# Optimization experiments

Hardware: AMD Instinct MI355X
Metric: run time of the kernel (lower is better)

## Reference

```python
import jax, jax.numpy as jnp
import numpy as np

INPUT_SIZE = 1024
HIDDEN = 4096
NUM_BLOCKS = 8
BLOCK = HIDDEN // NUM_BLOCKS  # 512
T, B = 64, 256


def setup_inputs() -> dict:
    key = jax.random.key(0)
    ks = jax.random.split(key, 5)
    stdv = 1.0 / np.sqrt(HIDDEN)
    x = jax.random.normal(ks[0], (T, B, INPUT_SIZE), dtype=jnp.float32)
    h_0 = jnp.zeros((B, HIDDEN), dtype=jnp.float32)
    # nn.Linear(input_size, 3*hidden): weight (3H, in), bias (3H)
    W_i_w = jax.random.uniform(ks[1], (3 * HIDDEN, INPUT_SIZE), minval=-stdv, maxval=stdv, dtype=jnp.float32)
    W_i_b = jax.random.uniform(ks[2], (3 * HIDDEN,), minval=-stdv, maxval=stdv, dtype=jnp.float32)
    # per-block nn.Linear(block, 3*block, bias=False): weight (3s, s), stacked (nb, 3s, s)
    W_h = jax.random.uniform(ks[3], (NUM_BLOCKS, 3 * BLOCK, BLOCK), minval=-stdv, maxval=stdv, dtype=jnp.float32)
    b_h = jax.random.uniform(ks[4], (3 * HIDDEN,), minval=-stdv, maxval=stdv, dtype=jnp.float32)
    return {"x": x, "h_0": h_0, "W_i_w": W_i_w, "W_i_b": W_i_b, "W_h": W_h, "b_h": b_h}


def reference(x, h_0, W_i_w, W_i_b, W_h, b_h):
    Tt, Bb, _ = x.shape
    H = b_h.shape[0] // 3
    nb = W_h.shape[0]
    s = H // nb
    # precompute input gates for all timesteps: (T, B, 3H)
    x_gates = jnp.einsum('tbi,gi->tbg', x, W_i_w) + W_i_b

    def step(h, xg):
        # block-diagonal recurrent transform; layout per block is [r_b, z_b, n_b] (3s),
        # concatenated over blocks -> (B, 3H) interleaved, matching torch cat order
        hb = h.reshape(Bb, nb, s)
        h_gates = jnp.einsum('bns,ngs->bng', hb, W_h).reshape(Bb, 3 * H) + b_h
        gates = xg + h_gates
        # torch chunk(3, dim=1) slices by H (mixes gate types across blocks -- faithful)
        r_t = jax.nn.sigmoid(gates[:, :H])
        z_t = jax.nn.sigmoid(gates[:, H:2 * H])
        h_n_gate = h_gates[:, 2 * H:]
        x_n_gate = xg[:, 2 * H:]
        n_t = jnp.tanh(x_n_gate + r_t * h_n_gate)
        h_new = (1.0 - z_t) * n_t + z_t * h
        return h_new, h_new

    h_T, output = jax.lax.scan(step, h_0, x_gates)
    return output, h_T
```

## Files before the change

### kernel.cpp

```cpp
#include <hip/hip_runtime.h>

#define T_STEPS 64
#define BATCH   256
#define IN_SZ   1024
#define HID     4096
#define BLK     512
#define GATES   12288
#define GROW    1536

#define BM 128
#define BN 128
#define BK 64

using bf16x8  = __attribute__((ext_vector_type(8))) __bf16;
using floatx4 = __attribute__((ext_vector_type(4))) float;
typedef const __attribute__((address_space(1))) unsigned int* gas_u32;
typedef __attribute__((address_space(3))) unsigned int* las_u32;

__device__ __forceinline__ unsigned short f2bf(float f) {
    union { float f; unsigned int u; } v; v.f = f;
    unsigned int u = v.u;
    unsigned int r = (u + 0x7fffu + ((u >> 16) & 1u)) >> 16;
    return (unsigned short)r;
}

__global__ __launch_bounds__(256) void cast_f32_bf16(
    const float* __restrict__ in, unsigned short* __restrict__ out, int n4)
{
    int i = blockIdx.x * 256 + threadIdx.x;
    if (i >= n4) return;
    float4 v = reinterpret_cast<const float4*>(in)[i];
    ushort4 o;
    o.x = f2bf(v.x); o.y = f2bf(v.y); o.z = f2bf(v.z); o.w = f2bf(v.w);
    reinterpret_cast<ushort4*>(out)[i] = o;
}

__global__ __launch_bounds__(256) void init_h(
    const float* __restrict__ h0, float* __restrict__ hT,
    unsigned short* __restrict__ hbf, int n)
{
    int i = blockIdx.x * 256 + threadIdx.x;
    if (i >= n) return;
    float v = h0[i];
    hT[i] = v;
    hbf[i] = f2bf(v);
}

__global__ __launch_bounds__(256, 2) void gemm_abt(
    const unsigned short* __restrict__ Ag,
    const unsigned short* __restrict__ Bg,
    float* __restrict__ C,
    int lda, int K, int nt_count, int blockdiag)
{
    __shared__ unsigned short lsA[BM * BK];
    __shared__ unsigned short lsB[BN * BK];

    const int bx = blockIdx.x;
    const int mt = bx / nt_count;
    const int nt = bx - mt * nt_count;
    const int m0 = mt * BM;
    const int n0 = nt * BN;

    const int tid  = threadIdx.x;
    const int wave = tid >> 6;
    const int lane = tid & 63;
    const int q    = lane >> 4;
    const int l16  = lane & 15;
    const int wm   = (wave >> 1) * 64;
    const int wn   = (wave & 1) * 64;

    const int a_col0 = blockdiag ? (n0 / GROW) * BLK : 0;

    floatx4 acc[4][4];
    #pragma unroll
    for (int mf = 0; mf < 4; mf++)
        #pragma unroll
        for (int nf = 0; nf < 4; nf++)
            acc[mf][nf] = floatx4{0.0f, 0.0f, 0.0f, 0.0f};

    for (int k0 = 0; k0 < K; k0 += BK) {
        __syncthreads();
        #pragma unroll
        for (int i = 0; i < 4; i++) {
            const int seg = wave * 4 + i;
            const int g   = seg * 64 + lane;
            const int row = g >> 3;
            const int cs  = ((g & 7) ^ (row & 7)) << 3;
            const unsigned short* ga = Ag + (size_t)(m0 + row) * lda + a_col0 + k0 + cs;
            __builtin_amdgcn_global_load_lds((gas_u32)ga,
                (las_u32)&lsA[seg * 512 + lane * 8], 16, 0, 0);
            const unsigned short* gb = Bg + (size_t)(n0 + row) * (size_t)K + k0 + cs;
            __builtin_amdgcn_global_load_lds((gas_u32)gb,
                (las_u32)&lsB[seg * 512 + lane * 8], 16, 0, 0);
        }
        __syncthreads();

        #pragma unroll
        for (int ks = 0; ks < BK; ks += 32) {
            bf16x8 a[4], b[4];
            #pragma unroll
            for (int mf = 0; mf < 4; mf++) {
                const int row = wm + mf * 16 + l16;
                const int pb  = ((ks >> 3) + q) ^ (row & 7);
                a[mf] = *reinterpret_cast<const bf16x8*>(&lsA[row * BK + pb * 8]);
            }
            #pragma unroll
            for (int nf = 0; nf < 4; nf++) {
                const int row = wn + nf * 16 + l16;
                const int pb  = ((ks >> 3) + q) ^ (row & 7);
                b[nf] = *reinterpret_cast<const bf16x8*>(&lsB[row * BK + pb * 8]);
            }
            #pragma unroll
            for (int mf = 0; mf < 4; mf++)
                #pragma unroll
                for (int nf = 0; nf < 4; nf++)
                    acc[mf][nf] = __builtin_amdgcn_mfma_f32_16x16x32_bf16(
                        a[mf], b[nf], acc[mf][nf], 0, 0, 0);
        }
    }

    #pragma unroll
    for (int mf = 0; mf < 4; mf++) {
        const int mrow0 = m0 + wm + mf * 16 + q * 4;
        #pragma unroll
        for (int nf = 0; nf < 4; nf++) {
            const int col = n0 + wn + nf * 16 + l16;
            #pragma unroll
            for (int r = 0; r < 4; r++)
                C[(size_t)(mrow0 + r) * GATES + col] = acc[mf][nf][r];
        }
    }
}

__global__ __launch_bounds__(256) void pointwise(
    const float* __restrict__ xgb, const float* __restrict__ hgb,
    const float* __restrict__ wib, const float* __restrict__ bh,
    float* __restrict__ hT, float* __restrict__ out,
    unsigned short* __restrict__ hbf)
{
    int gid = blockIdx.x * 256 + threadIdx.x;
    int b = gid >> 12;
    int i = gid & 4095;
    size_t base = (size_t)b * GATES;

    float g_r  = (xgb[base + i]        + wib[i])        + (hgb[base + i]        + bh[i]);
    float g_z  = (xgb[base + HID + i]  + wib[HID + i])  + (hgb[base + HID + i]  + bh[HID + i]);
    float x_n  =  xgb[base + 2*HID + i] + wib[2*HID + i];
    float h_n  =  hgb[base + 2*HID + i] + bh[2*HID + i];

    float r = 1.0f / (1.0f + __expf(-g_r));
    float z = 1.0f / (1.0f + __expf(-g_z));
    float n = tanhf(x_n + r * h_n);

    size_t hi = (size_t)b * HID + i;
    float h_old = hT[hi];
    float h_new = (1.0f - z) * n + z * h_old;
    hT[hi]  = h_new;
    out[hi] = h_new;
    hbf[hi] = f2bf(h_new);
}

extern "C" void kernel_launch(void* const* d_in, const int* in_sizes, int n_in,
                              void* d_out, int out_size, void* d_ws, size_t ws_size,
                              hipStream_t stream)
{
    const float* x   = (const float*)d_in[0];
    const float* h0  = (const float*)d_in[1];
    const float* Wi  = (const float*)d_in[2];
    const float* Wib = (const float*)d_in[3];
    const float* Wh  = (const float*)d_in[4];
    const float* bh  = (const float*)d_in[5];

    float* out = (float*)d_out;
    float* hT  = out + (size_t)T_STEPS * BATCH * HID;

    float* xg_all        = (float*)d_ws;
    unsigned short* x_bf = (unsigned short*)(xg_all + (size_t)T_STEPS * BATCH * GATES);
    unsigned short* wi_bf = x_bf  + (size_t)T_STEPS * BATCH * IN_SZ;
    unsigned short* wh_bf = wi_bf + (size_t)GATES * IN_SZ;
    unsigned short* h_bf  = wh_bf + (size_t)GATES * BLK;
    float* hgb = (float*)(h_bf + (size_t)BATCH * HID);

    const int n_x  = T_STEPS * BATCH * IN_SZ;
    const int n_wi = GATES * IN_SZ;
    const int n_wh = GATES * BLK;

    cast_f32_bf16<<<(n_x / 4 + 255) / 256, 256, 0, stream>>>(x,  x_bf,  n_x / 4);
    cast_f32_bf16<<<(n_wi / 4 + 255) / 256, 256, 0, stream>>>(Wi, wi_bf, n_wi / 4);
    cast_f32_bf16<<<(n_wh / 4 + 255) / 256, 256, 0, stream>>>(Wh, wh_bf, n_wh / 4);
    init_h<<<(BATCH * HID + 255) / 256, 256, 0, stream>>>(h0, hT, h_bf, BATCH * HID);

    gemm_abt<<<(T_STEPS * BATCH / BM) * (GATES / BN), 256, 0, stream>>>(
        x_bf, wi_bf, xg_all, IN_SZ, IN_SZ, GATES / BN, 0);

    for (int t = 0; t < T_STEPS; t++) {
        gemm_abt<<<(BATCH / BM) * (GATES / BN), 256, 0, stream>>>(
            h_bf, wh_bf, hgb, HID, BLK, GATES / BN, 1);
        pointwise<<<BATCH * HID / 256, 256, 0, stream>>>(
            xg_all + (size_t)t * BATCH * GATES, hgb, Wib, bh,
            hT, out + (size_t)t * BATCH * HID, h_bf);
    }
}
```

Before: 2.124 ms.

## Fuse recurrent block-diagonal GEMM with GRU pointwise update per timestep

Replaces the per-step recurrent GEMM plus separate pointwise kernel with one fused kernel. Each workgroup computes the r, z and n gate tiles for 64 batch rows by 64 hidden columns, then applies the GRU update directly from the accumulators. This removes the round-trip of the full hidden-gate tensor through global memory and one launch per step. The hidden state in bf16 is ping-ponged between two buffers so that blocks reading h do not race with blocks writing it. Costs: each gate phase loads full 512-deep tiles into 128 KB of shared memory with no overlap between loads and MFMA work, and the h tile is reloaded once per gate.

```diff
diff --git a/kernel.cpp b/kernel.cpp
--- a/kernel.cpp
+++ b/kernel.cpp
@@ -11,6 +11,9 @@
 #define BM 128
 #define BN 128
 #define BK 64
+
+#define BMT 64
+#define CN  64
 
 using bf16x8  = __attribute__((ext_vector_type(8))) __bf16;
 using floatx4 = __attribute__((ext_vector_type(4))) float;
@@ -132,32 +135,123 @@
     }
 }
 
-__global__ __launch_bounds__(256) void pointwise(
-    const float* __restrict__ xgb, const float* __restrict__ hgb,
-    const float* __restrict__ wib, const float* __restrict__ bh,
-    float* __restrict__ hT, float* __restrict__ out,
-    unsigned short* __restrict__ hbf)
-{
-    int gid = blockIdx.x * 256 + threadIdx.x;
-    int b = gid >> 12;
-    int i = gid & 4095;
-    size_t base = (size_t)b * GATES;
-
-    float g_r  = (xgb[base + i]        + wib[i])        + (hgb[base + i]        + bh[i]);
-    float g_z  = (xgb[base + HID + i]  + wib[HID + i])  + (hgb[base + HID + i]  + bh[HID + i]);
-    float x_n  =  xgb[base + 2*HID + i] + wib[2*HID + i];
-    float h_n  =  hgb[base + 2*HID + i] + bh[2*HID + i];
-
-    float r = 1.0f / (1.0f + __expf(-g_r));
-    float z = 1.0f / (1.0f + __expf(-g_z));
-    float n = tanhf(x_n + r * h_n);
-
-    size_t hi = (size_t)b * HID + i;
-    float h_old = hT[hi];
-    float h_new = (1.0f - z) * n + z * h_old;
-    hT[hi]  = h_new;
-    out[hi] = h_new;
-    hbf[hi] = f2bf(h_new);
+__global__ __launch_bounds__(256) void fused_step(
+    const unsigned short* __restrict__ hbf_in,
+    const unsigned short* __restrict__ Whb,
+    const float* __restrict__ xg,
+    const float* __restrict__ wib,
+    const float* __restrict__ bh,
+    float* __restrict__ hT,
+    float* __restrict__ out,
+    unsigned short* __restrict__ hbf_out)
+{
+    __shared__ unsigned short lsA[BMT * BLK];
+    __shared__ unsigned short lsB[CN * BLK];
+
+    const int bid  = blockIdx.x;
+    const int cidx = bid & 63;
+    const int bidx = bid >> 6;
+    const int b0   = bidx * BMT;
+    const int c0   = cidx * CN;
+
+    const int tid  = threadIdx.x;
+    const int lane = tid & 63;
+    const int wave = tid >> 6;
+    const int q    = lane >> 4;
+    const int l16  = lane & 15;
+    const int wm   = (wave >> 1) * 32;
+    const int wn   = (wave & 1) * 32;
+
+    floatx4 accR[2][2], accZ[2][2], accN[2][2];
+    #pragma unroll
+    for (int mf = 0; mf < 2; mf++)
+        #pragma unroll
+        for (int nf = 0; nf < 2; nf++) {
+            accR[mf][nf] = floatx4{0.f, 0.f, 0.f, 0.f};
+            accZ[mf][nf] = floatx4{0.f, 0.f, 0.f, 0.f};
+            accN[mf][nf] = floatx4{0.f, 0.f, 0.f, 0.f};
+        }
+
+    #define GATE_BODY(G, ACC)                                                        \
+    {                                                                                \
+        const int gbase = (G) * HID;                                                 \
+        const int nb    = (gbase + c0) / GROW;                                       \
+        const int acol0 = nb * BLK;                                                  \
+        const unsigned short* Bbase = Whb + (size_t)(gbase + c0) * BLK;              \
+        __syncthreads();       \
+        _Pragma("unroll")                                                            \
+        for (int it = 0; it < 16; it++) {                                            \
+            const int gc  = it * 256 + tid;                                          \
+            const int row = gc >> 6;                                                 \
+            const int kb  = (gc & 63) ^ (row & 7);                                   \
+            const unsigned short* ga =                                               \
+                hbf_in + (size_t)(b0 + row) * HID + acol0 + kb * 8;                  \
+            __builtin_amdgcn_global_load_lds((gas_u32)ga,                            \
+                (las_u32)&lsA[gc * 8], 16, 0, 0);                                    \
+            const unsigned short* gb = Bbase + (size_t)row * BLK + kb * 8;           \
+            __builtin_amdgcn_global_load_lds((gas_u32)gb,                            \
+                (las_u32)&lsB[gc * 8], 16, 0, 0);                                    \
+        }                                                                            \
+        __syncthreads();                \
+        _Pragma("unroll")                                                            \
+        for (int ks = 0; ks < BLK; ks += 32) {                                       \
+            bf16x8 a[2], b[2];                                                       \
+            _Pragma("unroll")                                                        \
+            for (int mf = 0; mf < 2; mf++) {                                         \
+                const int row = wm + mf * 16 + l16;                                  \
+                const int pb  = ((ks >> 3) + q) ^ (row & 7);                         \
+                a[mf] = *reinterpret_cast<const bf16x8*>(&lsA[row * BLK + pb * 8]);  \
+            }                                                                        \
+            _Pragma("unroll")                                                        \
+            for (int nf = 0; nf < 2; nf++) {                                         \
+                const int row = wn + nf * 16 + l16;                                  \
+                const int pb  = ((ks >> 3) + q) ^ (row & 7);                         \
+                b[nf] = *reinterpret_cast<const bf16x8*>(&lsB[row * BLK + pb * 8]);  \
+            }                                                                        \
+            _Pragma("unroll")                                                        \
+            for (int mf = 0; mf < 2; mf++)                                           \
+                _Pragma("unroll")                                                    \
+                for (int nf = 0; nf < 2; nf++)                                       \
+                    ACC[mf][nf] = __builtin_amdgcn_mfma_f32_16x16x32_bf16(           \
+                        a[mf], b[nf], ACC[mf][nf], 0, 0, 0);                         \
+        }                                                                            \
+    }
+
+    GATE_BODY(0, accR)
+    GATE_BODY(1, accZ)
+    GATE_BODY(2, accN)
+    #undef GATE_BODY
+
+    #pragma unroll
+    for (int nf = 0; nf < 2; nf++) {
+        const int i   = c0 + wn + nf * 16 + l16;
+        const float br  = wib[i] + bh[i];
+        const float bz  = wib[HID + i] + bh[HID + i];
+        const float bxn = wib[2 * HID + i];
+        const float bhn = bh[2 * HID + i];
+        #pragma unroll
+        for (int mf = 0; mf < 2; mf++) {
+            const int m0r = b0 + wm + mf * 16 + q * 4;
+            #pragma unroll
+            for (int r = 0; r < 4; r++) {
+                const int m = m0r + r;
+                const size_t xb = (size_t)m * GATES;
+                const float gr = xg[xb + i]           + br  + accR[mf][nf][r];
+                const float gz = xg[xb + HID + i]     + bz  + accZ[mf][nf][r];
+                const float xn = xg[xb + 2 * HID + i] + bxn;
+                const float hn = accN[mf][nf][r]      + bhn;
+                const float rr = 1.0f / (1.0f + __expf(-gr));
+                const float zz = 1.0f / (1.0f + __expf(-gz));
+                const float nn = tanhf(xn + rr * hn);
+                const size_t hi = (size_t)m * HID + i;
+                const float ho = hT[hi];
+                const float hnew = (1.0f - zz) * nn + zz * ho;
+                hT[hi]      = hnew;
+                out[hi]     = hnew;
+                hbf_out[hi] = f2bf(hnew);
+            }
+        }
+    }
 }
 
 extern "C" void kernel_launch(void* const* d_in, const int* in_sizes, int n_in,
@@ -178,8 +272,8 @@
     unsigned short* x_bf = (unsigned short*)(xg_all + (size_t)T_STEPS * BATCH * GATES);
     unsigned short* wi_bf = x_bf  + (size_t)T_STEPS * BATCH * IN_SZ;
     unsigned short* wh_bf = wi_bf + (size_t)GATES * IN_SZ;
-    unsigned short* h_bf  = wh_bf + (size_t)GATES * BLK;
-    float* hgb = (float*)(h_bf + (size_t)BATCH * HID);
+    unsigned short* hbf0  = wh_bf + (size_t)GATES * BLK;
+    unsigned short* hbf1  = hbf0  + (size_t)BATCH * HID;
 
     const int n_x  = T_STEPS * BATCH * IN_SZ;
     const int n_wi = GATES * IN_SZ;
@@ -188,16 +282,16 @@
     cast_f32_bf16<<<(n_x / 4 + 255) / 256, 256, 0, stream>>>(x,  x_bf,  n_x / 4);
     cast_f32_bf16<<<(n_wi / 4 + 255) / 256, 256, 0, stream>>>(Wi, wi_bf, n_wi / 4);
     cast_f32_bf16<<<(n_wh / 4 + 255) / 256, 256, 0, stream>>>(Wh, wh_bf, n_wh / 4);
-    init_h<<<(BATCH * HID + 255) / 256, 256, 0, stream>>>(h0, hT, h_bf, BATCH * HID);
+    init_h<<<(BATCH * HID + 255) / 256, 256, 0, stream>>>(h0, hT, hbf0, BATCH * HID);
 
     gemm_abt<<<(T_STEPS * BATCH / BM) * (GATES / BN), 256, 0, stream>>>(
         x_bf, wi_bf, xg_all, IN_SZ, IN_SZ, GATES / BN, 0);
 
     for (int t = 0; t < T_STEPS; t++) {
-        gemm_abt<<<(BATCH / BM) * (GATES / BN), 256, 0, stream>>>(
-            h_bf, wh_bf, hgb, HID, BLK, GATES / BN, 1);
-        pointwise<<<BATCH * HID / 256, 256, 0, stream>>>(
-            xg_all + (size_t)t * BATCH * GATES, hgb, Wib, bh,
-            hT, out + (size_t)t * BATCH * HID, h_bf);
-    }
-}
+        fused_step<<<(BATCH / BMT) * (HID / CN), 256, 0, stream>>>(
+            (t & 1) ? hbf1 : hbf0, wh_bf,
+            xg_all + (size_t)t * BATCH * GATES, Wib, bh,
+            hT, out + (size_t)t * BATCH * HID,
+            (t & 1) ? hbf0 : hbf1);
+    }
+}
```

Result: no change. 2.124 ms (+0.0%).

## Replace per-timestep GEMM and pointwise launches with a persistent fused GRU kernel

Applied to the files above, without the earlier changes.

Swaps the 128 per-step kernel launches (a recurrent GEMM plus a pointwise kernel each step) for one persistent kernel of 256 workgroups. Each workgroup computes the r, z and n gate tiles for a 64x64 slice of hidden state with double-buffered LDS staging, then applies the gate nonlinearities in registers and keeps h in registers across steps. A global atomic barrier separates timesteps, and ping-pong bf16 h buffers replace the fp32 hgb round trip. This removes launch overhead and the intermediate gate traffic, but relies on all 256 workgroups being resident at once and adds grid-barrier latency each step.

```diff
diff --git a/kernel.cpp b/kernel.cpp
--- a/kernel.cpp
+++ b/kernel.cpp
@@ -12,6 +12,9 @@
 #define BN 128
 #define BK 64
 
+#define BMT 64
+#define CN  64
+
 using bf16x8  = __attribute__((ext_vector_type(8))) __bf16;
 using floatx4 = __attribute__((ext_vector_type(4))) float;
 typedef const __attribute__((address_space(1))) unsigned int* gas_u32;
@@ -36,21 +39,24 @@
 }
 
 __global__ __launch_bounds__(256) void init_h(
-    const float* __restrict__ h0, float* __restrict__ hT,
-    unsigned short* __restrict__ hbf, int n)
+    const float* __restrict__ h0, unsigned short* __restrict__ hbf, int n)
 {
     int i = blockIdx.x * 256 + threadIdx.x;
     if (i >= n) return;
-    float v = h0[i];
-    hT[i] = v;
-    hbf[i] = f2bf(v);
+    hbf[i] = f2bf(h0[i]);
+}
+
+__global__ __launch_bounds__(64) void zero_u32(unsigned int* p, int n)
+{
+    int i = blockIdx.x * 64 + threadIdx.x;
+    if (i < n) p[i] = 0u;
 }
 
 __global__ __launch_bounds__(256, 2) void gemm_abt(
     const unsigned short* __restrict__ Ag,
     const unsigned short* __restrict__ Bg,
     float* __restrict__ C,
-    int lda, int K, int nt_count, int blockdiag)
+    int lda, int K, int nt_count)
 {
     __shared__ unsigned short lsA[BM * BK];
     __shared__ unsigned short lsB[BN * BK];
@@ -69,8 +75,6 @@
     const int wm   = (wave >> 1) * 64;
     const int wn   = (wave & 1) * 64;
 
-    const int a_col0 = blockdiag ? (n0 / GROW) * BLK : 0;
-
     floatx4 acc[4][4];
     #pragma unroll
     for (int mf = 0; mf < 4; mf++)
@@ -86,7 +90,7 @@
             const int g   = seg * 64 + lane;
             const int row = g >> 3;
             const int cs  = ((g & 7) ^ (row & 7)) << 3;
-            const unsigned short* ga = Ag + (size_t)(m0 + row) * lda + a_col0 + k0 + cs;
+            const unsigned short* ga = Ag + (size_t)(m0 + row) * lda + k0 + cs;
             __builtin_amdgcn_global_load_lds((gas_u32)ga,
                 (las_u32)&lsA[seg * 512 + lane * 8], 16, 0, 0);
             const unsigned short* gb = Bg + (size_t)(n0 + row) * (size_t)K + k0 + cs;
@@ -132,32 +136,213 @@
     }
 }
 
-__global__ __launch_bounds__(256) void pointwise(
-    const float* __restrict__ xgb, const float* __restrict__ hgb,
-    const float* __restrict__ wib, const float* __restrict__ bh,
-    float* __restrict__ hT, float* __restrict__ out,
-    unsigned short* __restrict__ hbf)
-{
-    int gid = blockIdx.x * 256 + threadIdx.x;
-    int b = gid >> 12;
-    int i = gid & 4095;
-    size_t base = (size_t)b * GATES;
-
-    float g_r  = (xgb[base + i]        + wib[i])        + (hgb[base + i]        + bh[i]);
-    float g_z  = (xgb[base + HID + i]  + wib[HID + i])  + (hgb[base + HID + i]  + bh[HID + i]);
-    float x_n  =  xgb[base + 2*HID + i] + wib[2*HID + i];
-    float h_n  =  hgb[base + 2*HID + i] + bh[2*HID + i];
-
-    float r = 1.0f / (1.0f + __expf(-g_r));
-    float z = 1.0f / (1.0f + __expf(-g_z));
-    float n = tanhf(x_n + r * h_n);
-
-    size_t hi = (size_t)b * HID + i;
-    float h_old = hT[hi];
-    float h_new = (1.0f - z) * n + z * h_old;
-    hT[hi]  = h_new;
-    out[hi] = h_new;
-    hbf[hi] = f2bf(h_new);
+__device__ __forceinline__ void stage_tile(
+    const unsigned short* ap, const unsigned short* bp,
+    unsigned short* la, unsigned short* lb, int tid)
+{
+    #pragma unroll
+    for (int it = 0; it < 8; ++it) {
+        __builtin_amdgcn_global_load_lds((gas_u32)(ap + it * 8 * HID),
+            (las_u32)(la + (it * 256 + tid) * 8), 16, 0, 0);
+        __builtin_amdgcn_global_load_lds((gas_u32)(bp + it * 8 * BLK),
+            (las_u32)(lb + (it * 256 + tid) * 8), 16, 0, 0);
+    }
+}
+
+__device__ __forceinline__ void gemm_chunk(
+    const unsigned short* la, const unsigned short* lb,
+    int wm, int wn, int q, int l16, floatx4 (&acc)[2][2])
+{
+    #pragma unroll
+    for (int ks = 0; ks < 256; ks += 32) {
+        bf16x8 a[2], b[2];
+        #pragma unroll
+        for (int mf = 0; mf < 2; mf++) {
+            const int row = wm + mf * 16 + l16;
+            const int pb  = ((ks >> 3) + q) ^ (row & 7);
+            a[mf] = *reinterpret_cast<const bf16x8*>(&la[row * 256 + pb * 8]);
+        }
+        #pragma unroll
+        for (int nf = 0; nf < 2; nf++) {
+            const int row = wn + nf * 16 + l16;
+            const int pb  = ((ks >> 3) + q) ^ (row & 7);
+            b[nf] = *reinterpret_cast<const bf16x8*>(&lb[row * 256 + pb * 8]);
+        }
+        #pragma unroll
+        for (int mf = 0; mf < 2; mf++)
+            #pragma unroll
+            for (int nf = 0; nf < 2; nf++)
+                acc[mf][nf] = __builtin_amdgcn_mfma_f32_16x16x32_bf16(
+                    a[mf], b[nf], acc[mf][nf], 0, 0, 0);
+    }
+}
+
+__device__ __forceinline__ void grid_barrier(unsigned int* cnt, unsigned int target)
+{
+    __threadfence();
+    __syncthreads();
+    if (threadIdx.x == 0) {
+        __hip_atomic_fetch_add(cnt, 1u, __ATOMIC_RELEASE, __HIP_MEMORY_SCOPE_AGENT);
+        while (__hip_atomic_load(cnt, __ATOMIC_RELAXED, __HIP_MEMORY_SCOPE_AGENT) < target)
+            __builtin_amdgcn_s_sleep(2);
+    }
+    __syncthreads();
+    __threadfence();
+}
+
+__global__ __launch_bounds__(256, 1) void persistent_gru(
+    unsigned short* hbfA,
+    unsigned short* hbfB,
+    const unsigned short* __restrict__ Whb,
+    const float* __restrict__ xg_all,
+    const float* __restrict__ wib,
+    const float* __restrict__ bh,
+    const float* __restrict__ h0,
+    float* __restrict__ hT,
+    float* __restrict__ out,
+    unsigned int* barrier_cnt)
+{
+    __shared__ unsigned short ls[2][2][64 * 256];
+
+    const int bid  = blockIdx.x;
+    const int g7   = bid & 7;
+    const int s    = bid >> 3;
+    const int cidx = g7 * 8 + (s & 7);
+    const int bidx = s >> 3;
+    const int b0   = bidx * BMT;
+    const int c0   = cidx * CN;
+
+    const int tid  = threadIdx.x;
+    const int lane = tid & 63;
+    const int wave = tid >> 6;
+    const int q    = lane >> 4;
+    const int l16  = lane & 15;
+    const int wm   = (wave >> 1) * 32;
+    const int wn   = (wave & 1) * 32;
+
+    const int krow = tid >> 5;
+    const int kb   = (tid & 31) ^ (krow & 7);
+
+    const int acol0 = ((0 * HID + c0) / GROW) * BLK;
+    const int acol1 = ((1 * HID + c0) / GROW) * BLK;
+    const int acol2 = ((2 * HID + c0) / GROW) * BLK;
+    const unsigned short* bb0 = Whb + (size_t)(0 * HID + c0 + krow) * BLK + kb * 8;
+    const unsigned short* bb1 = Whb + (size_t)(1 * HID + c0 + krow) * BLK + kb * 8;
+    const unsigned short* bb2 = Whb + (size_t)(2 * HID + c0 + krow) * BLK + kb * 8;
+
+    float br[2], bz[2], bxn[2], bhn[2];
+    #pragma unroll
+    for (int nf = 0; nf < 2; nf++) {
+        const int i = c0 + wn + nf * 16 + l16;
+        br[nf]  = wib[i]           + bh[i];
+        bz[nf]  = wib[HID + i]     + bh[HID + i];
+        bxn[nf] = wib[2 * HID + i];
+        bhn[nf] = bh[2 * HID + i];
+    }
+
+    float hreg[2][2][4];
+    #pragma unroll
+    for (int mf = 0; mf < 2; mf++)
+        #pragma unroll
+        for (int nf = 0; nf < 2; nf++)
+            #pragma unroll
+            for (int r = 0; r < 4; r++) {
+                const int m = b0 + wm + mf * 16 + q * 4 + r;
+                const int i = c0 + wn + nf * 16 + l16;
+                hreg[mf][nf][r] = h0[(size_t)m * HID + i];
+            }
+
+    for (int t = 0; t < T_STEPS; t++) {
+        const unsigned short* hin = (t & 1) ? hbfB : hbfA;
+        unsigned short*      hout = (t & 1) ? hbfA : hbfB;
+        const float* xgt = xg_all + (size_t)t * BATCH * GATES;
+        float* outt = out + (size_t)t * BATCH * HID;
+
+        const unsigned short* abase = hin + (size_t)(b0 + krow) * HID + kb * 8;
+
+        floatx4 aR[2][2], aZ[2][2], aN[2][2];
+        #pragma unroll
+        for (int mf = 0; mf < 2; mf++)
+            #pragma unroll
+            for (int nf = 0; nf < 2; nf++) {
+                aR[mf][nf] = floatx4{0.f, 0.f, 0.f, 0.f};
+                aZ[mf][nf] = floatx4{0.f, 0.f, 0.f, 0.f};
+                aN[mf][nf] = floatx4{0.f, 0.f, 0.f, 0.f};
+            }
+
+        stage_tile(abase + acol0, bb0, &ls[0][0][0], &ls[0][1][0], tid);
+
+        float xpre[3][2][2][4];
+        #pragma unroll
+        for (int g = 0; g < 3; g++)
+            #pragma unroll
+            for (int mf = 0; mf < 2; mf++)
+                #pragma unroll
+                for (int r = 0; r < 4; r++) {
+                    const size_t xb = (size_t)(b0 + wm + mf * 16 + q * 4 + r) * GATES + g * HID;
+                    #pragma unroll
+                    for (int nf = 0; nf < 2; nf++)
+                        xpre[g][mf][nf][r] = xgt[xb + c0 + wn + nf * 16 + l16];
+                }
+        __syncthreads();
+
+        stage_tile(abase + acol0 + 256, bb0 + 256, &ls[1][0][0], &ls[1][1][0], tid);
+        gemm_chunk(&ls[0][0][0], &ls[0][1][0], wm, wn, q, l16, aR);
+        __syncthreads();
+
+        stage_tile(abase + acol1, bb1, &ls[0][0][0], &ls[0][1][0], tid);
+        gemm_chunk(&ls[1][0][0], &ls[1][1][0], wm, wn, q, l16, aR);
+        __syncthreads();
+
+        stage_tile(abase + acol1 + 256, bb1 + 256, &ls[1][0][0], &ls[1][1][0], tid);
+        gemm_chunk(&ls[0][0][0], &ls[0][1][0], wm, wn, q, l16, aZ);
+        __syncthreads();
+
+        stage_tile(abase + acol2, bb2, &ls[0][0][0], &ls[0][1][0], tid);
+        gemm_chunk(&ls[1][0][0], &ls[1][1][0], wm, wn, q, l16, aZ);
+        __syncthreads();
+
+        stage_tile(abase + acol2 + 256, bb2 + 256, &ls[1][0][0], &ls[1][1][0], tid);
+        gemm_chunk(&ls[0][0][0], &ls[0][1][0], wm, wn, q, l16, aN);
+        __syncthreads();
+
+        gemm_chunk(&ls[1][0][0], &ls[1][1][0], wm, wn, q, l16, aN);
+
+        #pragma unroll
+        for (int mf = 0; mf < 2; mf++)
+            #pragma unroll
+            for (int nf = 0; nf < 2; nf++)
+                #pragma unroll
+                for (int r = 0; r < 4; r++) {
+                    const float gr = xpre[0][mf][nf][r] + br[nf]  + aR[mf][nf][r];
+                    const float gz = xpre[1][mf][nf][r] + bz[nf]  + aZ[mf][nf][r];
+                    const float xn = xpre[2][mf][nf][r] + bxn[nf];
+                    const float hn = aN[mf][nf][r] + bhn[nf];
+                    const float rr = 1.0f / (1.0f + __expf(-gr));
+                    const float zz = 1.0f / (1.0f + __expf(-gz));
+                    const float nn = tanhf(xn + rr * hn);
+                    const float hnew = (1.0f - zz) * nn + zz * hreg[mf][nf][r];
+                    hreg[mf][nf][r] = hnew;
+                    const int m = b0 + wm + mf * 16 + q * 4 + r;
+                    const int i = c0 + wn + nf * 16 + l16;
+                    const size_t hi = (size_t)m * HID + i;
+                    outt[hi] = hnew;
+                    hout[hi] = f2bf(hnew);
+                }
+
+        grid_barrier(barrier_cnt, (unsigned int)(t + 1) * 256u);
+    }
+
+    #pragma unroll
+    for (int mf = 0; mf < 2; mf++)
+        #pragma unroll
+        for (int nf = 0; nf < 2; nf++)
+            #pragma unroll
+            for (int r = 0; r < 4; r++) {
+                const int m = b0 + wm + mf * 16 + q * 4 + r;
+                const int i = c0 + wn + nf * 16 + l16;
+                hT[(size_t)m * HID + i] = hreg[mf][nf][r];
+            }
 }
 
 extern "C" void kernel_launch(void* const* d_in, const int* in_sizes, int n_in,
@@ -174,12 +359,13 @@
     float* out = (float*)d_out;
     float* hT  = out + (size_t)T_STEPS * BATCH * HID;
 
-    float* xg_all        = (float*)d_ws;
-    unsigned short* x_bf = (unsigned short*)(xg_all + (size_t)T_STEPS * BATCH * GATES);
+    float* xg_all         = (float*)d_ws;
+    unsigned short* x_bf  = (unsigned short*)(xg_all + (size_t)T_STEPS * BATCH * GATES);
     unsigned short* wi_bf = x_bf  + (size_t)T_STEPS * BATCH * IN_SZ;
     unsigned short* wh_bf = wi_bf + (size_t)GATES * IN_SZ;
-    unsigned short* h_bf  = wh_bf + (size_t)GATES * BLK;
-    float* hgb = (float*)(h_bf + (size_t)BATCH * HID);
+    unsigned short* hbf0  = wh_bf + (size_t)GATES * BLK;
+    unsigned short* hbf1  = hbf0  + (size_t)BATCH * HID;
+    unsigned int* bar_cnt = (unsigned int*)(hbf1 + (size_t)BATCH * HID);
 
     const int n_x  = T_STEPS * BATCH * IN_SZ;
     const int n_wi = GATES * IN_SZ;
@@ -188,16 +374,12 @@
     cast_f32_bf16<<<(n_x / 4 + 255) / 256, 256, 0, stream>>>(x,  x_bf,  n_x / 4);
     cast_f32_bf16<<<(n_wi / 4 + 255) / 256, 256, 0, stream>>>(Wi, wi_bf, n_wi / 4);
     cast_f32_bf16<<<(n_wh / 4 + 255) / 256, 256, 0, stream>>>(Wh, wh_bf, n_wh / 4);
-    init_h<<<(BATCH * HID + 255) / 256, 256, 0, stream>>>(h0, hT, h_bf, BATCH * HID);
+    init_h<<<(BATCH * HID + 255) / 256, 256, 0, stream>>>(h0, hbf0, BATCH * HID);
+    zero_u32<<<1, 64, 0, stream>>>(bar_cnt, 1);
 
     gemm_abt<<<(T_STEPS * BATCH / BM) * (GATES / BN), 256, 0, stream>>>(
-        x_bf, wi_bf, xg_all, IN_SZ, IN_SZ, GATES / BN, 0);
-
-    for (int t = 0; t < T_STEPS; t++) {
-        gemm_abt<<<(BATCH / BM) * (GATES / BN), 256, 0, stream>>>(
-            h_bf, wh_bf, hgb, HID, BLK, GATES / BN, 1);
-        pointwise<<<BATCH * HID / 256, 256, 0, stream>>>(
-            xg_all + (size_t)t * BATCH * GATES, hgb, Wib, bh,
-            hT, out + (size_t)t * BATCH * HID, h_bf);
-    }
-}
+        x_bf, wi_bf, xg_all, IN_SZ, IN_SZ, GATES / BN);
+
+    persistent_gru<<<dim3(256), dim3(256), 0, stream>>>(
+        hbf0, hbf1, wh_bf, xg_all, Wib, bh, h0, hT, out, bar_cnt);
+}
```

Measured after the change: 5.037 ms. 137% more time.
